# Optimization experiments

Hardware: AMD Instinct MI355X
Metric: run time of the kernel (lower is better)

The kernel has to match this reference:

```python
import jax, jax.numpy as jnp
import numpy as np

N, D, R, E, H = 100000, 128, 4, 150000, 8
DK = D // H  # 16


def setup_inputs() -> dict:
    key = jax.random.key(0)
    ks = jax.random.split(key, 12)
    w_scale = 1.0 / np.sqrt(D)
    rel_scale = 1.0 / np.sqrt(DK)
    return {
        'x': jax.random.normal(ks[0], (N, D), dtype=jnp.float32),
        'edges_src': jax.random.randint(ks[1], (R, E), 0, N, dtype=jnp.int32),
        'edges_dst': jax.random.randint(ks[2], (R, E), 0, N, dtype=jnp.int32),
        'Wk': jax.random.normal(ks[3], (D, D), dtype=jnp.float32) * w_scale,
        'bk': jnp.zeros((D,), dtype=jnp.float32),
        'Wq': jax.random.normal(ks[4], (D, D), dtype=jnp.float32) * w_scale,
        'bq': jnp.zeros((D,), dtype=jnp.float32),
        'Wv': jax.random.normal(ks[5], (D, D), dtype=jnp.float32) * w_scale,
        'bv': jnp.zeros((D,), dtype=jnp.float32),
        'Wa': jax.random.normal(ks[6], (D, D), dtype=jnp.float32) * w_scale,
        'ba': jnp.zeros((D,), dtype=jnp.float32),
        'rel_att': jax.random.normal(ks[7], (R, H, DK, DK), dtype=jnp.float32) * rel_scale,
        'rel_msg': jax.random.normal(ks[8], (R, H, DK, DK), dtype=jnp.float32) * rel_scale,
        'rel_pri': jnp.ones((R, H), dtype=jnp.float32),
        'skip': jnp.ones((1,), dtype=jnp.float32),
    }


def reference(x, edges_src, edges_dst, Wk, bk, Wq, bq, Wv, bv, Wa, ba,
              rel_att, rel_msg, rel_pri, skip):
    n, d = x.shape
    r, e = edges_src.shape
    h, dk = rel_att.shape[1], rel_att.shape[2]
    sqrt_dk = jnp.sqrt(jnp.asarray(dk, dtype=x.dtype))

    # per-type k/q/v projections (single node type) -> [N, H, dk]
    k = (x @ Wk.T + bk).reshape(n, h, dk)
    q = (x @ Wq.T + bq).reshape(n, h, dk)
    v = (x @ Wv.T + bv).reshape(n, h, dk)

    # edge_attention: per-relation per-head dk x dk transforms on gathered src feats
    key_e = jnp.einsum('rehd,rhdf->rehf', k[edges_src], rel_att)   # [R,E,H,dk]
    att = (q[edges_dst] * key_e).sum(-1) * rel_pri[:, None, :] / sqrt_dk  # [R,E,H]
    val = jnp.einsum('rehd,rhdf->rehf', v[edges_src], rel_msg)     # [R,E,H,dk]

    # mailbox softmax per (relation, dst node, head) via segment ops
    seg = (edges_dst.astype(jnp.int32) + jnp.arange(r, dtype=jnp.int32)[:, None] * n).reshape(-1)
    att_f = att.reshape(r * e, h)
    m = jax.ops.segment_max(att_f, seg, num_segments=r * n)
    a = jnp.exp(att_f - m[seg])
    s = jax.ops.segment_sum(a, seg, num_segments=r * n)
    attn = a / s[seg]                                              # [R*E, H]

    # softmax-weighted scatter aggregation -> [R, N, H*dk]
    msg = (attn[:, :, None] * val.reshape(r * e, h, dk)).reshape(r * e, h * dk)
    t = jax.ops.segment_sum(msg, seg, num_segments=r * n).reshape(r, n, d)
    t = t.mean(axis=0)  # cross_reducer='mean' over relations

    # skip-gated output linear (dropout is identity in eval)
    alpha = jax.nn.sigmoid(skip[0])
    return (t @ Wa.T + ba) * alpha + x * (1.0 - alpha)
```

## Files before the change

### kernel.cpp

```cpp
#include <hip/hip_runtime.h>

#define NN 100000
#define DD 128
#define RR 4
#define EE 150000
#define HH 8
#define DK 16

#define NSEG (RR * NN)
#define NEDGE (RR * EE)
#define SCAN_BLK 256
#define SCAN_ELEMS 1024
#define SCAN_NB ((NSEG + SCAN_ELEMS - 1) / SCAN_ELEMS)
#define PAD_K 136
#define MAT_U 132
#define ND2 (NN * 64)

typedef short bf16x8 __attribute__((ext_vector_type(8)));
typedef float f32x4  __attribute__((ext_vector_type(4)));

__device__ __forceinline__ unsigned short f2bf(float f) {
    unsigned u = __float_as_uint(f);
    return (unsigned short)((u + 0x7fffu + ((u >> 16) & 1u)) >> 16);
}
__device__ __forceinline__ float bflo(unsigned w) { return __uint_as_float(w << 16); }
__device__ __forceinline__ float bfhi(unsigned w) { return __uint_as_float(w & 0xffff0000u); }

__global__ __launch_bounds__(128) void prep_wmsg(
    const float* __restrict__ Wv, const float* __restrict__ bv,
    const float* __restrict__ rel_msg,
    float* __restrict__ Wm, float* __restrict__ bm)
{
    const int b = blockIdx.x;
    const int r = b >> 3, h = b & 7;
    const int c = threadIdx.x;
    __shared__ float Msh[256];
    for (int i = c; i < 256; i += 128) Msh[i] = rel_msg[(b << 8) + i];
    __syncthreads();

    #pragma unroll 4
    for (int f = 0; f < 16; ++f) {
        float acc = 0.f;
        #pragma unroll
        for (int d = 0; d < 16; ++d)
            acc = __builtin_fmaf(Msh[d * 16 + f], Wv[(h * 16 + d) * DD + c], acc);
        Wm[((long)r * DD + h * 16 + f) * DD + c] = acc;
    }
    if (c < 16) {
        float acc = 0.f;
        #pragma unroll
        for (int d = 0; d < 16; ++d)
            acc = __builtin_fmaf(Msh[d * 16 + c], bv[h * 16 + d], acc);
        bm[r * DD + h * 16 + c] = acc;
    }
}

__global__ __launch_bounds__(256) void mfma_proj(
    const float* __restrict__ X,
    const float* __restrict__ Wk, const float* __restrict__ Wq, const float* __restrict__ Wm,
    const float* __restrict__ bk, const float* __restrict__ bq, const float* __restrict__ bm,
    unsigned* __restrict__ kb, unsigned* __restrict__ qb, unsigned* __restrict__ vMb)
{
    const int tid = threadIdx.x;
    const int lane = tid & 63;
    const int wave = tid >> 6;
    const int wr = wave >> 1;
    const int wc = wave & 1;
    const long m0 = (long)blockIdx.x * 64;
    const int mat = blockIdx.y;
    const float* W    = (mat == 0) ? Wk : (mat == 1) ? Wq : (Wm + (long)(mat - 2) * DD * DD);
    const float* bias = (mat == 0) ? bk : (mat == 1) ? bq : (bm + (mat - 2) * DD);
    unsigned* out     = (mat == 0) ? kb : (mat == 1) ? qb : (vMb + (long)(mat - 2) * ND2);

    __shared__ short Xs[64 * PAD_K];
    __shared__ short Wsh[128 * PAD_K];

    #pragma unroll
    for (int i = 0; i < 8; ++i) {
        int f = tid + 256 * i;
        int row = f >> 5, c4 = f & 31;
        long m = m0 + row;
        float4 v = make_float4(0.f, 0.f, 0.f, 0.f);
        if (m < NN) v = ((const float4*)(X + m * DD))[c4];
        unsigned u0 = (unsigned)f2bf(v.x) | ((unsigned)f2bf(v.y) << 16);
        unsigned u1 = (unsigned)f2bf(v.z) | ((unsigned)f2bf(v.w) << 16);
        *(uint2*)&Xs[row * PAD_K + c4 * 4] = make_uint2(u0, u1);
    }
    #pragma unroll
    for (int i = 0; i < 16; ++i) {
        int f = tid + 256 * i;
        int row = f >> 5, c4 = f & 31;
        float4 v = ((const float4*)(W + row * DD))[c4];
        unsigned u0 = (unsigned)f2bf(v.x) | ((unsigned)f2bf(v.y) << 16);
        unsigned u1 = (unsigned)f2bf(v.z) | ((unsigned)f2bf(v.w) << 16);
        *(uint2*)&Wsh[row * PAD_K + c4 * 4] = make_uint2(u0, u1);
    }
    __syncthreads();

    const int lrow = lane & 15;
    const int kg = lane >> 4;

    f32x4 acc[2][4];
    #pragma unroll
    for (int i = 0; i < 2; ++i)
        #pragma unroll
        for (int j = 0; j < 4; ++j) acc[i][j] = (f32x4){0.f, 0.f, 0.f, 0.f};

    #pragma unroll
    for (int ks = 0; ks < 4; ++ks) {
        const int kk = ks * 32 + kg * 8;
        bf16x8 xf[2], wf[4];
        #pragma unroll
        for (int i = 0; i < 2; ++i)
            xf[i] = *(const bf16x8*)&Xs[(wr * 32 + i * 16 + lrow) * PAD_K + kk];
        #pragma unroll
        for (int j = 0; j < 4; ++j)
            wf[j] = *(const bf16x8*)&Wsh[(wc * 64 + j * 16 + lrow) * PAD_K + kk];
        #pragma unroll
        for (int i = 0; i < 2; ++i)
            #pragma unroll
            for (int j = 0; j < 4; ++j)
                acc[i][j] = __builtin_amdgcn_mfma_f32_16x16x32_bf16(wf[j], xf[i], acc[i][j], 0, 0, 0);
    }

    #pragma unroll
    for (int j = 0; j < 4; ++j) {
        const int nb = wc * 64 + j * 16 + kg * 4;
        const float b0 = bias[nb + 0], b1 = bias[nb + 1];
        const float b2 = bias[nb + 2], b3 = bias[nb + 3];
        #pragma unroll
        for (int i = 0; i < 2; ++i) {
            long m = m0 + wr * 32 + i * 16 + lrow;
            if (m < NN) {
                unsigned u0 = (unsigned)f2bf(acc[i][j][0] + b0) | ((unsigned)f2bf(acc[i][j][1] + b1) << 16);
                unsigned u1 = (unsigned)f2bf(acc[i][j][2] + b2) | ((unsigned)f2bf(acc[i][j][3] + b3) << 16);
                *(uint2*)&out[m * 64 + (nb >> 1)] = make_uint2(u0, u1);
            }
        }
    }
}

__global__ __launch_bounds__(256) void mfma_out(
    const float* __restrict__ T, const float* __restrict__ Wa, const float* __restrict__ ba,
    float* __restrict__ out, const float* __restrict__ skip, const float* __restrict__ xres)
{
    const int tid = threadIdx.x;
    const int lane = tid & 63;
    const int wave = tid >> 6;
    const int wr = wave >> 1;
    const int wc = wave & 1;
    const long m0 = (long)blockIdx.x * 64;

    __shared__ short Xs[64 * PAD_K];
    __shared__ short Wsh[128 * PAD_K];

    #pragma unroll
    for (int i = 0; i < 8; ++i) {
        int f = tid + 256 * i;
        int row = f >> 5, c4 = f & 31;
        long m = m0 + row;
        float4 v = make_float4(0.f, 0.f, 0.f, 0.f);
        if (m < NN) v = ((const float4*)(T + m * DD))[c4];
        unsigned u0 = (unsigned)f2bf(v.x * 0.25f) | ((unsigned)f2bf(v.y * 0.25f) << 16);
        unsigned u1 = (unsigned)f2bf(v.z * 0.25f) | ((unsigned)f2bf(v.w * 0.25f) << 16);
        *(uint2*)&Xs[row * PAD_K + c4 * 4] = make_uint2(u0, u1);
    }
    #pragma unroll
    for (int i = 0; i < 16; ++i) {
        int f = tid + 256 * i;
        int row = f >> 5, c4 = f & 31;
        float4 v = ((const float4*)(Wa + row * DD))[c4];
        unsigned u0 = (unsigned)f2bf(v.x) | ((unsigned)f2bf(v.y) << 16);
        unsigned u1 = (unsigned)f2bf(v.z) | ((unsigned)f2bf(v.w) << 16);
        *(uint2*)&Wsh[row * PAD_K + c4 * 4] = make_uint2(u0, u1);
    }
    __syncthreads();

    const int lrow = lane & 15;
    const int kg = lane >> 4;

    f32x4 acc[2][4];
    #pragma unroll
    for (int i = 0; i < 2; ++i)
        #pragma unroll
        for (int j = 0; j < 4; ++j) acc[i][j] = (f32x4){0.f, 0.f, 0.f, 0.f};

    #pragma unroll
    for (int ks = 0; ks < 4; ++ks) {
        const int kk = ks * 32 + kg * 8;
        bf16x8 xf[2], wf[4];
        #pragma unroll
        for (int i = 0; i < 2; ++i)
            xf[i] = *(const bf16x8*)&Xs[(wr * 32 + i * 16 + lrow) * PAD_K + kk];
        #pragma unroll
        for (int j = 0; j < 4; ++j)
            wf[j] = *(const bf16x8*)&Wsh[(wc * 64 + j * 16 + lrow) * PAD_K + kk];
        #pragma unroll
        for (int i = 0; i < 2; ++i)
            #pragma unroll
            for (int j = 0; j < 4; ++j)
                acc[i][j] = __builtin_amdgcn_mfma_f32_16x16x32_bf16(xf[i], wf[j], acc[i][j], 0, 0, 0);
    }

    const float s = 1.f / (1.f + __expf(-skip[0]));
    const float al = s, bt = 1.f - s;

    #pragma unroll
    for (int j = 0; j < 4; ++j) {
        const int n = wc * 64 + j * 16 + lrow;
        const float bcol = ba[n];
        #pragma unroll
        for (int i = 0; i < 2; ++i) {
            #pragma unroll
            for (int r = 0; r < 4; ++r) {
                long m = m0 + wr * 32 + i * 16 + kg * 4 + r;
                if (m < NN) {
                    long o = m * DD + n;
                    out[o] = __builtin_fmaf(xres[o], bt, (acc[i][j][r] + bcol) * al);
                }
            }
        }
    }
}


__global__ __launch_bounds__(256) void csr_hist(
    const int* __restrict__ edst, int* __restrict__ cnt)
{
    int idx = blockIdx.x * 256 + threadIdx.x;
    if (idx >= NEDGE) return;
    int r = idx / EE;
    atomicAdd(&cnt[r * NN + edst[idx]], 1);
}

__global__ __launch_bounds__(SCAN_BLK) void scan1(
    const int* __restrict__ cnt, int* __restrict__ offs, int* __restrict__ bsum)
{
    __shared__ int sh[SCAN_BLK];
    int blk = blockIdx.x, tid = threadIdx.x;
    int base = blk * SCAN_ELEMS + tid * 4;
    int v0 = 0, v1 = 0, v2 = 0, v3 = 0;
    if (base + 3 < NSEG) {
        int4 t = *(const int4*)(cnt + base);
        v0 = t.x; v1 = t.y; v2 = t.z; v3 = t.w;
    } else {
        if (base + 0 < NSEG) v0 = cnt[base + 0];
        if (base + 1 < NSEG) v1 = cnt[base + 1];
        if (base + 2 < NSEG) v2 = cnt[base + 2];
        if (base + 3 < NSEG) v3 = cnt[base + 3];
    }
    int tsum = v0 + v1 + v2 + v3;
    sh[tid] = tsum;
    __syncthreads();
    #pragma unroll
    for (int d = 1; d < SCAN_BLK; d <<= 1) {
        int x = (tid >= d) ? sh[tid - d] : 0;
        __syncthreads();
        sh[tid] += x;
        __syncthreads();
    }
    int excl = sh[tid] - tsum;
    int r0 = excl, r1 = r0 + v0, r2 = r1 + v1, r3 = r2 + v2;
    if (base + 3 < NSEG) {
        *(int4*)(offs + base) = make_int4(r0, r1, r2, r3);
    } else {
        if (base + 0 < NSEG) offs[base + 0] = r0;
        if (base + 1 < NSEG) offs[base + 1] = r1;
        if (base + 2 < NSEG) offs[base + 2] = r2;
        if (base + 3 < NSEG) offs[base + 3] = r3;
    }
    if (tid == SCAN_BLK - 1) bsum[blk] = sh[tid];
}

__global__ __launch_bounds__(512) void scan2(int* __restrict__ bsum)
{
    __shared__ int sh[512];
    int tid = threadIdx.x;
    int v = (tid < SCAN_NB) ? bsum[tid] : 0;
    sh[tid] = v;
    __syncthreads();
    #pragma unroll
    for (int d = 1; d < 512; d <<= 1) {
        int x = (tid >= d) ? sh[tid - d] : 0;
        __syncthreads();
        sh[tid] += x;
        __syncthreads();
    }
    if (tid < SCAN_NB) bsum[tid] = sh[tid] - v;
}

__global__ __launch_bounds__(SCAN_BLK) void scan3(
    int* __restrict__ offs, int* __restrict__ cur, const int* __restrict__ bsum)
{
    int blk = blockIdx.x;
    int add = bsum[blk];
    int base = blk * SCAN_ELEMS + threadIdx.x * 4;
    #pragma unroll
    for (int j = 0; j < 4; ++j)
        if (base + j < NSEG) {
            int v = offs[base + j] + add;
            offs[base + j] = v;
            cur[base + j] = v;
        }
}

__global__ __launch_bounds__(256) void csr_fill(
    const int* __restrict__ esrc, const int* __restrict__ edst,
    int* __restrict__ cur, int* __restrict__ csr_src)
{
    int idx = blockIdx.x * 256 + threadIdx.x;
    if (idx >= NEDGE) return;
    int r = idx / EE;
    int pos = atomicAdd(&cur[r * NN + edst[idx]], 1);
    csr_src[pos] = esrc[idx];
}

#define GT 512
__global__ __launch_bounds__(GT) void gather_agg(
    const unsigned* __restrict__ kb, const unsigned* __restrict__ qbuf,
    const unsigned* __restrict__ vMb,
    const int* __restrict__ csr_src, const int* __restrict__ offs,
    const float* __restrict__ rel_att, const float* __restrict__ rel_pri,
    float* __restrict__ t)
{
    __shared__ unsigned As[32 * MAT_U];
    __shared__ float prish[32];
    const int tid = threadIdx.x;
    #pragma unroll
    for (int i = 0; i < (32 * 128) / GT; ++i) {
        int f = tid + GT * i;
        int m = f >> 7, j = f & 127;
        float2 a = *(const float2*)(rel_att + m * 256 + j * 2);
        As[m * MAT_U + j] = (unsigned)f2bf(a.x) | ((unsigned)f2bf(a.y) << 16);
    }
    if (tid < 32) prish[tid] = rel_pri[tid] * 0.25f;
    __syncthreads();

    int gidx = blockIdx.x * GT + tid;
    if (gidx >= NN * HH) return;
    const int dst = gidx >> 3, h = gidx & 7;

    float qh[16];
    {
        const uint4* qp = (const uint4*)(qbuf + (long)dst * 64 + h * 8);
        uint4 qa = qp[0], qc = qp[1];
        qh[0] = bflo(qa.x);  qh[1] = bfhi(qa.x);
        qh[2] = bflo(qa.y);  qh[3] = bfhi(qa.y);
        qh[4] = bflo(qa.z);  qh[5] = bfhi(qa.z);
        qh[6] = bflo(qa.w);  qh[7] = bfhi(qa.w);
        qh[8] = bflo(qc.x);  qh[9] = bfhi(qc.x);
        qh[10] = bflo(qc.y); qh[11] = bfhi(qc.y);
        qh[12] = bflo(qc.z); qh[13] = bfhi(qc.z);
        qh[14] = bflo(qc.w); qh[15] = bfhi(qc.w);
    }

    float tacc[16];
    #pragma unroll
    for (int f = 0; f < 16; ++f) tacc[f] = 0.f;

    for (int r = 0; r < RR; ++r) {
        const int seg = r * NN + dst;
        const int beg = offs[seg];
        const int end = (seg == NSEG - 1) ? NEDGE : offs[seg + 1];
        if (end <= beg) continue;

        const unsigned* A = &As[(r * HH + h) * MAT_U];
        const float pri = prish[r * HH + h];

        float qbar[16];
        #pragma unroll
        for (int d = 0; d < 16; ++d) {
            uint4 r0 = *(const uint4*)&A[d * 8];
            uint4 r1 = *(const uint4*)&A[d * 8 + 4];
            float acc = bflo(r0.x) * qh[0];
            acc = __builtin_fmaf(bfhi(r0.x), qh[1], acc);
            acc = __builtin_fmaf(bflo(r0.y), qh[2], acc);
            acc = __builtin_fmaf(bfhi(r0.y), qh[3], acc);
            acc = __builtin_fmaf(bflo(r0.z), qh[4], acc);
            acc = __builtin_fmaf(bfhi(r0.z), qh[5], acc);
            acc = __builtin_fmaf(bflo(r0.w), qh[6], acc);
            acc = __builtin_fmaf(bfhi(r0.w), qh[7], acc);
            acc = __builtin_fmaf(bflo(r1.x), qh[8], acc);
            acc = __builtin_fmaf(bfhi(r1.x), qh[9], acc);
            acc = __builtin_fmaf(bflo(r1.y), qh[10], acc);
            acc = __builtin_fmaf(bfhi(r1.y), qh[11], acc);
            acc = __builtin_fmaf(bflo(r1.z), qh[12], acc);
            acc = __builtin_fmaf(bfhi(r1.z), qh[13], acc);
            acc = __builtin_fmaf(bflo(r1.w), qh[14], acc);
            acc = __builtin_fmaf(bfhi(r1.w), qh[15], acc);
            qbar[d] = acc * pri;
        }

        float s = 0.f;
        float vb[16];
        #pragma unroll
        for (int f = 0; f < 16; ++f) vb[f] = 0.f;

        const unsigned* vMr = vMb + (long)r * ND2;
        for (int e = beg; e < end; ++e) {
            int src = csr_src[e];
            const uint4* kp = (const uint4*)(kb + (long)src * 64 + h * 8);
            uint4 ka = kp[0], kc = kp[1];
            const uint4* vp = (const uint4*)(vMr + (long)src * 64 + h * 8);
            uint4 va = vp[0], vc = vp[1];

            float att;
            att  = bflo(ka.x) * qbar[0];
            att = __builtin_fmaf(bfhi(ka.x), qbar[1], att);
            att = __builtin_fmaf(bflo(ka.y), qbar[2], att);
            att = __builtin_fmaf(bfhi(ka.y), qbar[3], att);
            att = __builtin_fmaf(bflo(ka.z), qbar[4], att);
            att = __builtin_fmaf(bfhi(ka.z), qbar[5], att);
            att = __builtin_fmaf(bflo(ka.w), qbar[6], att);
            att = __builtin_fmaf(bfhi(ka.w), qbar[7], att);
            att = __builtin_fmaf(bflo(kc.x), qbar[8], att);
            att = __builtin_fmaf(bfhi(kc.x), qbar[9], att);
            att = __builtin_fmaf(bflo(kc.y), qbar[10], att);
            att = __builtin_fmaf(bfhi(kc.y), qbar[11], att);
            att = __builtin_fmaf(bflo(kc.z), qbar[12], att);
            att = __builtin_fmaf(bfhi(kc.z), qbar[13], att);
            att = __builtin_fmaf(bflo(kc.w), qbar[14], att);
            att = __builtin_fmaf(bfhi(kc.w), qbar[15], att);

            float ea = __expf(att);
            s += ea;
            vb[0]  = __builtin_fmaf(ea, bflo(va.x), vb[0]);
            vb[1]  = __builtin_fmaf(ea, bfhi(va.x), vb[1]);
            vb[2]  = __builtin_fmaf(ea, bflo(va.y), vb[2]);
            vb[3]  = __builtin_fmaf(ea, bfhi(va.y), vb[3]);
            vb[4]  = __builtin_fmaf(ea, bflo(va.z), vb[4]);
            vb[5]  = __builtin_fmaf(ea, bfhi(va.z), vb[5]);
            vb[6]  = __builtin_fmaf(ea, bflo(va.w), vb[6]);
            vb[7]  = __builtin_fmaf(ea, bfhi(va.w), vb[7]);
            vb[8]  = __builtin_fmaf(ea, bflo(vc.x), vb[8]);
            vb[9]  = __builtin_fmaf(ea, bfhi(vc.x), vb[9]);
            vb[10] = __builtin_fmaf(ea, bflo(vc.y), vb[10]);
            vb[11] = __builtin_fmaf(ea, bfhi(vc.y), vb[11]);
            vb[12] = __builtin_fmaf(ea, bflo(vc.z), vb[12]);
            vb[13] = __builtin_fmaf(ea, bfhi(vc.z), vb[13]);
            vb[14] = __builtin_fmaf(ea, bflo(vc.w), vb[14]);
            vb[15] = __builtin_fmaf(ea, bfhi(vc.w), vb[15]);
        }

        float inv = 1.f / s;
        #pragma unroll
        for (int f = 0; f < 16; ++f)
            tacc[f] = __builtin_fmaf(vb[f], inv, tacc[f]);
    }

    float* tp = t + (long)dst * DD + h * DK;
    #pragma unroll
    for (int i = 0; i < 4; ++i) {
        float4 o;
        o.x = tacc[4*i]; o.y = tacc[4*i+1]; o.z = tacc[4*i+2]; o.w = tacc[4*i+3];
        *(float4*)(tp + 4 * i) = o;
    }
}

extern "C" void kernel_launch(void* const* d_in, const int* in_sizes, int n_in,
                              void* d_out, int out_size, void* d_ws, size_t ws_size,
                              hipStream_t stream)
{
    const float* x   = (const float*)d_in[0];
    const int* esrc  = (const int*)d_in[1];
    const int* edst  = (const int*)d_in[2];
    const float* Wk  = (const float*)d_in[3];
    const float* bk  = (const float*)d_in[4];
    const float* Wq  = (const float*)d_in[5];
    const float* bq  = (const float*)d_in[6];
    const float* Wv  = (const float*)d_in[7];
    const float* bv  = (const float*)d_in[8];
    const float* Wa  = (const float*)d_in[9];
    const float* ba  = (const float*)d_in[10];
    const float* rel_att = (const float*)d_in[11];
    const float* rel_msg = (const float*)d_in[12];
    const float* rel_pri = (const float*)d_in[13];
    const float* skip    = (const float*)d_in[14];
    float* out = (float*)d_out;

    float* ws = (float*)d_ws;
    const long ND = (long)NN * DD;
    float* tbuf = ws;
    unsigned* qb  = (unsigned*)(ws + ND);
    unsigned* kb  = qb + ND2;
    unsigned* vMb = kb + ND2;
    float* Wm = (float*)(vMb + 4L * ND2);
    float* bm = Wm + 4 * DD * DD;
    int* cnt  = (int*)(bm + 512);
    int* offs = cnt + NSEG;
    int* cur  = offs + NSEG;
    int* bsum = cur + NSEG;
    int* csr  = bsum + 512;

    hipMemsetAsync(cnt, 0, NSEG * sizeof(int), stream);

    prep_wmsg<<<32, 128, 0, stream>>>(Wv, bv, rel_msg, Wm, bm);

    const int gb = (NN + 63) / 64;
    mfma_proj<<<dim3(gb, 6), 256, 0, stream>>>(x, Wk, Wq, Wm, bk, bq, bm, kb, qb, vMb);

    const int ebk = (NEDGE + 255) / 256;
    csr_hist<<<ebk, 256, 0, stream>>>(edst, cnt);
    scan1<<<SCAN_NB, SCAN_BLK, 0, stream>>>(cnt, offs, bsum);
    scan2<<<1, 512, 0, stream>>>(bsum);
    scan3<<<SCAN_NB, SCAN_BLK, 0, stream>>>(offs, cur, bsum);
    csr_fill<<<ebk, 256, 0, stream>>>(esrc, edst, cur, csr);

    gather_agg<<<(NN * HH + GT - 1) / GT, GT, 0, stream>>>(
        kb, qb, vMb, csr, offs, rel_att, rel_pri, tbuf);

    mfma_out<<<gb, 256, 0, stream>>>(tbuf, Wa, ba, out, skip, x);
}
```

Measured before the change: 335.2 us.

## Prepack all projection weights to bf16 and loop six matrices per X tile

```diff
diff --git a/kernel.cpp b/kernel.cpp
--- a/kernel.cpp
+++ b/kernel.cpp
@@ -15,6 +15,7 @@
 #define PAD_K 136
 #define MAT_U 132
 #define ND2 (NN * 64)
+#define WMAT 8192
 
 typedef short bf16x8 __attribute__((ext_vector_type(8)));
 typedef float f32x4  __attribute__((ext_vector_type(4)));
@@ -26,15 +27,35 @@
 __device__ __forceinline__ float bflo(unsigned w) { return __uint_as_float(w << 16); }
 __device__ __forceinline__ float bfhi(unsigned w) { return __uint_as_float(w & 0xffff0000u); }
 
+__global__ __launch_bounds__(256) void prep_pack(
+    const float* __restrict__ Wk, const float* __restrict__ bk,
+    const float* __restrict__ Wq, const float* __restrict__ bq,
+    unsigned* __restrict__ wAll, float* __restrict__ bAll)
+{
+    const int b = blockIdx.x;
+    const float* W = b ? Wq : Wk;
+    const float* bias = b ? bq : bk;
+    unsigned* out = wAll + b * WMAT;
+    const int tid = threadIdx.x;
+    #pragma unroll
+    for (int i = 0; i < 32; ++i) {
+        int idx = tid + 256 * i;
+        float2 v = *(const float2*)(W + idx * 2);
+        out[idx] = (unsigned)f2bf(v.x) | ((unsigned)f2bf(v.y) << 16);
+    }
+    if (tid < 128) bAll[b * 128 + tid] = bias[tid];
+}
+
 __global__ __launch_bounds__(128) void prep_wmsg(
     const float* __restrict__ Wv, const float* __restrict__ bv,
     const float* __restrict__ rel_msg,
-    float* __restrict__ Wm, float* __restrict__ bm)
+    unsigned* __restrict__ wAll, float* __restrict__ bAll)
 {
     const int b = blockIdx.x;
     const int r = b >> 3, h = b & 7;
     const int c = threadIdx.x;
     __shared__ float Msh[256];
+    __shared__ float sh2[16][128];
     for (int i = c; i < 256; i += 128) Msh[i] = rel_msg[(b << 8) + i];
     __syncthreads();
 
@@ -44,21 +65,30 @@
         #pragma unroll
         for (int d = 0; d < 16; ++d)
             acc = __builtin_fmaf(Msh[d * 16 + f], Wv[(h * 16 + d) * DD + c], acc);
-        Wm[((long)r * DD + h * 16 + f) * DD + c] = acc;
+        sh2[f][c] = acc;
     }
     if (c < 16) {
         float acc = 0.f;
         #pragma unroll
         for (int d = 0; d < 16; ++d)
             acc = __builtin_fmaf(Msh[d * 16 + c], bv[h * 16 + d], acc);
-        bm[r * DD + h * 16 + c] = acc;
+        bAll[(2 + r) * 128 + h * 16 + c] = acc;
+    }
+    __syncthreads();
+
+    unsigned* out = wAll + (2 + r) * WMAT;
+    #pragma unroll
+    for (int k = 0; k < 8; ++k) {
+        int idx = c * 8 + k;
+        int f = idx >> 6, j = idx & 63;
+        unsigned u = (unsigned)f2bf(sh2[f][2 * j]) | ((unsigned)f2bf(sh2[f][2 * j + 1]) << 16);
+        out[(h * 16 + f) * 64 + j] = u;
     }
 }
 
 __global__ __launch_bounds__(256) void mfma_proj(
     const float* __restrict__ X,
-    const float* __restrict__ Wk, const float* __restrict__ Wq, const float* __restrict__ Wm,
-    const float* __restrict__ bk, const float* __restrict__ bq, const float* __restrict__ bm,
+    const unsigned* __restrict__ wAll, const float* __restrict__ bAll,
     unsigned* __restrict__ kb, unsigned* __restrict__ qb, unsigned* __restrict__ vMb)
 {
     const int tid = threadIdx.x;
@@ -67,13 +97,8 @@
     const int wr = wave >> 1;
     const int wc = wave & 1;
     const long m0 = (long)blockIdx.x * 64;
-    const int mat = blockIdx.y;
-    const float* W    = (mat == 0) ? Wk : (mat == 1) ? Wq : (Wm + (long)(mat - 2) * DD * DD);
-    const float* bias = (mat == 0) ? bk : (mat == 1) ? bq : (bm + (mat - 2) * DD);
-    unsigned* out     = (mat == 0) ? kb : (mat == 1) ? qb : (vMb + (long)(mat - 2) * ND2);
 
     __shared__ short Xs[64 * PAD_K];
-    __shared__ short Wsh[128 * PAD_K];
 
     #pragma unroll
     for (int i = 0; i < 8; ++i) {
@@ -86,55 +111,56 @@
         unsigned u1 = (unsigned)f2bf(v.z) | ((unsigned)f2bf(v.w) << 16);
         *(uint2*)&Xs[row * PAD_K + c4 * 4] = make_uint2(u0, u1);
     }
-    #pragma unroll
-    for (int i = 0; i < 16; ++i) {
-        int f = tid + 256 * i;
-        int row = f >> 5, c4 = f & 31;
-        float4 v = ((const float4*)(W + row * DD))[c4];
-        unsigned u0 = (unsigned)f2bf(v.x) | ((unsigned)f2bf(v.y) << 16);
-        unsigned u1 = (unsigned)f2bf(v.z) | ((unsigned)f2bf(v.w) << 16);
-        *(uint2*)&Wsh[row * PAD_K + c4 * 4] = make_uint2(u0, u1);
-    }
     __syncthreads();
 
     const int lrow = lane & 15;
     const int kg = lane >> 4;
 
-    f32x4 acc[2][4];
-    #pragma unroll
-    for (int i = 0; i < 2; ++i)
-        #pragma unroll
-        for (int j = 0; j < 4; ++j) acc[i][j] = (f32x4){0.f, 0.f, 0.f, 0.f};
-
-    #pragma unroll
-    for (int ks = 0; ks < 4; ++ks) {
-        const int kk = ks * 32 + kg * 8;
-        bf16x8 xf[2], wf[4];
+    bf16x8 xf[4][2];
+    #pragma unroll
+    for (int ks = 0; ks < 4; ++ks)
         #pragma unroll
         for (int i = 0; i < 2; ++i)
-            xf[i] = *(const bf16x8*)&Xs[(wr * 32 + i * 16 + lrow) * PAD_K + kk];
-        #pragma unroll
-        for (int j = 0; j < 4; ++j)
-            wf[j] = *(const bf16x8*)&Wsh[(wc * 64 + j * 16 + lrow) * PAD_K + kk];
+            xf[ks][i] = *(const bf16x8*)&Xs[(wr * 32 + i * 16 + lrow) * PAD_K + ks * 32 + kg * 8];
+
+    #pragma unroll
+    for (int mat = 0; mat < 6; ++mat) {
+        const unsigned* Wp = wAll + mat * WMAT;
+        const float* bias = bAll + mat * 128;
+        unsigned* outb = (mat == 0) ? kb : (mat == 1) ? qb : (vMb + (long)(mat - 2) * ND2);
+
+        f32x4 acc[2][4];
         #pragma unroll
         for (int i = 0; i < 2; ++i)
             #pragma unroll
+            for (int j = 0; j < 4; ++j) acc[i][j] = (f32x4){0.f, 0.f, 0.f, 0.f};
+
+        #pragma unroll
+        for (int ks = 0; ks < 4; ++ks) {
+            bf16x8 wf[4];
+            #pragma unroll
             for (int j = 0; j < 4; ++j)
-                acc[i][j] = __builtin_amdgcn_mfma_f32_16x16x32_bf16(wf[j], xf[i], acc[i][j], 0, 0, 0);
-    }
-
-    #pragma unroll
-    for (int j = 0; j < 4; ++j) {
-        const int nb = wc * 64 + j * 16 + kg * 4;
-        const float b0 = bias[nb + 0], b1 = bias[nb + 1];
-        const float b2 = bias[nb + 2], b3 = bias[nb + 3];
-        #pragma unroll
-        for (int i = 0; i < 2; ++i) {
-            long m = m0 + wr * 32 + i * 16 + lrow;
-            if (m < NN) {
-                unsigned u0 = (unsigned)f2bf(acc[i][j][0] + b0) | ((unsigned)f2bf(acc[i][j][1] + b1) << 16);
-                unsigned u1 = (unsigned)f2bf(acc[i][j][2] + b2) | ((unsigned)f2bf(acc[i][j][3] + b3) << 16);
-                *(uint2*)&out[m * 64 + (nb >> 1)] = make_uint2(u0, u1);
+                wf[j] = *(const bf16x8*)(Wp + (wc * 64 + j * 16 + lrow) * 64 + ks * 16 + kg * 4);
+            #pragma unroll
+            for (int i = 0; i < 2; ++i)
+                #pragma unroll
+                for (int j = 0; j < 4; ++j)
+                    acc[i][j] = __builtin_amdgcn_mfma_f32_16x16x32_bf16(wf[j], xf[ks][i], acc[i][j], 0, 0, 0);
+        }
+
+        #pragma unroll
+        for (int j = 0; j < 4; ++j) {
+            const int nb = wc * 64 + j * 16 + kg * 4;
+            const float b0 = bias[nb + 0], b1 = bias[nb + 1];
+            const float b2 = bias[nb + 2], b3 = bias[nb + 3];
+            #pragma unroll
+            for (int i = 0; i < 2; ++i) {
+                long m = m0 + wr * 32 + i * 16 + lrow;
+                if (m < NN) {
+                    unsigned u0 = (unsigned)f2bf(acc[i][j][0] + b0) | ((unsigned)f2bf(acc[i][j][1] + b1) << 16);
+                    unsigned u1 = (unsigned)f2bf(acc[i][j][2] + b2) | ((unsigned)f2bf(acc[i][j][3] + b3) << 16);
+                    *(uint2*)&outb[m * 64 + (nb >> 1)] = make_uint2(u0, u1);
+                }
             }
         }
     }
@@ -484,9 +510,9 @@
     unsigned* qb  = (unsigned*)(ws + ND);
     unsigned* kb  = qb + ND2;
     unsigned* vMb = kb + ND2;
-    float* Wm = (float*)(vMb + 4L * ND2);
-    float* bm = Wm + 4 * DD * DD;
-    int* cnt  = (int*)(bm + 512);
+    unsigned* wAll = vMb + 4L * ND2;
+    float* bAll = (float*)(wAll + 6 * WMAT);
+    int* cnt  = (int*)(bAll + 768);
     int* offs = cnt + NSEG;
     int* cur  = offs + NSEG;
     int* bsum = cur + NSEG;
@@ -494,10 +520,11 @@
 
     hipMemsetAsync(cnt, 0, NSEG * sizeof(int), stream);
 
-    prep_wmsg<<<32, 128, 0, stream>>>(Wv, bv, rel_msg, Wm, bm);
+    prep_pack<<<2, 256, 0, stream>>>(Wk, bk, Wq, bq, wAll, bAll);
+    prep_wmsg<<<32, 128, 0, stream>>>(Wv, bv, rel_msg, wAll, bAll);
 
     const int gb = (NN + 63) / 64;
-    mfma_proj<<<dim3(gb, 6), 256, 0, stream>>>(x, Wk, Wq, Wm, bk, bq, bm, kb, qb, vMb);
+    mfma_proj<<<gb, 256, 0, stream>>>(x, wAll, bAll, kb, qb, vMb);
 
     const int ebk = (NEDGE + 255) / 256;
     csr_hist<<<ebk, 256, 0, stream>>>(edst, cnt);
```

Measured after the change: 349.2 us. 1.04x slower.
